# Kernel optimization log

Measured on AMD Instinct MI355X. Metric: run time of the kernel, lower is better.

Reference implementation:

```python
import math
import jax, jax.numpy as jnp
import numpy as np

D = 512
MEM_LEN = 1024
RATIO = 2


def setup_inputs() -> dict:
    key = jax.random.key(0)
    ks = jax.random.split(key, 16)
    s = 1.0 / math.sqrt(D)
    inp = {
        "x": jax.random.normal(ks[0], (4, 2048, D), jnp.float32),
        "fine_mem": jax.random.normal(ks[1], (8, 256, D), jnp.float32),
        "cmem_seq": jax.random.normal(ks[2], (16, 128, D), jnp.float32),
        "comp_query": jax.random.normal(ks[3], (D,), jnp.float32) * 0.02,
        "comp_W": jax.random.normal(ks[4], (D, D), jnp.float32) * s,
        "comp_b": jnp.zeros((D,), jnp.float32),
        "k_W": jax.random.normal(ks[5], (D, D), jnp.float32) * s,
        "k_b": jnp.zeros((D,), jnp.float32),
        "v_W": jax.random.normal(ks[6], (D, D), jnp.float32) * s,
        "v_b": jnp.zeros((D,), jnp.float32),
        "xk_W": jax.random.normal(ks[7], (D, D), jnp.float32) * s,
        "xk_b": jnp.zeros((D,), jnp.float32),
        "ck_W": jax.random.normal(ks[8], (D, D), jnp.float32) * s,
        "ck_b": jnp.zeros((D,), jnp.float32),
        "cv_W": jax.random.normal(ks[9], (D, D), jnp.float32) * s,
        "cv_b": jnp.zeros((D,), jnp.float32),
    }
    return inp


def _compress(combined, comp_query, comp_W, comp_b):
    # AttentionPoolCompressor, vectorized: L tokens -> L//RATIO pooled tokens
    L, d = combined.shape
    L_out = max(L // RATIO, 1)
    c = combined.reshape(L_out, RATIO, d)                      # [L_out, r, d]
    logits = jnp.einsum("d,lrd->lr", comp_query, c) * (d ** -0.5)
    w = jax.nn.softmax(logits, axis=-1)
    pooled = jnp.einsum("lr,lrd->ld", w, c)                    # [L_out, d]
    return pooled @ comp_W + comp_b


def _interp_linear(comp, L):
    # F.interpolate(mode='linear', align_corners=False) along length dim
    L_out = comp.shape[0]
    i = jnp.arange(L, dtype=jnp.float32)
    src = jnp.clip((i + 0.5) * (L_out / L) - 0.5, 0.0, L_out - 1)
    i0 = jnp.floor(src).astype(jnp.int32)
    i1 = jnp.minimum(i0 + 1, L_out - 1)
    frac = (src - i0)[:, None]
    return (1.0 - frac) * comp[i0] + frac * comp[i1]


def reference(x, fine_mem, cmem_seq, comp_query, comp_W, comp_b,
              k_W, k_b, v_W, v_b, xk_W, xk_b, ck_W, ck_b, cv_W, cv_b):
    B, S, d = x.shape
    Nf, Lm, _ = fine_mem.shape
    scale = d ** -0.5

    # keys/values over the ORIGINAL memories (projections precede eviction)
    fine_k = fine_mem @ k_W + k_b      # [Nf, Lm, d]
    fine_v = fine_mem @ v_W + v_b
    cmem_k = cmem_seq @ ck_W + ck_b    # [Nc, Lc, d]
    cmem_v = cmem_seq @ cv_W + cv_b

    # eviction: take leading chunks until cumsum >= mem_len/2 (static)
    K = min(int(math.ceil(0.5 * MEM_LEN / Lm)), Nf)
    combined = fine_mem[:K].reshape(K * Lm, d)                 # [L, d]
    compressed = _compress(combined, comp_query, comp_W, comp_b)
    decoded = _interp_linear(compressed, combined.shape[0])
    recon_loss = jnp.mean((decoded - combined) ** 2)

    # cross-attention over concatenated memory
    query = x @ xk_W + xk_b                                    # [B, S, d]
    mem_k = jnp.concatenate([fine_k.reshape(-1, d), cmem_k.reshape(-1, d)], 0)
    mem_v = jnp.concatenate([fine_v.reshape(-1, d), cmem_v.reshape(-1, d)], 0)
    scores = jnp.einsum("bsd,md->bsm", query, mem_k) * scale   # [B, S, M]
    attn = jax.nn.softmax(scores, axis=-1)
    mem_out = jnp.einsum("bsm,md->bsd", attn, mem_v)
    output = x + mem_out
    return (output, recon_loss)
```

## Files before the change

kernel.cpp:

```cpp
#include <hip/hip_runtime.h>

typedef __attribute__((ext_vector_type(8))) short bf16x8;
typedef __attribute__((ext_vector_type(4))) float f32x4;

#define MFMA16(a,b,c) __builtin_amdgcn_mfma_f32_16x16x32_bf16((a),(b),(c),0,0,0)

__device__ __forceinline__ unsigned short f2bf(float f) {
  unsigned int u = __builtin_bit_cast(unsigned int, f);
  u = (u + 0x7FFFu + ((u >> 16) & 1u)) >> 16;
  return (unsigned short)u;
}
__device__ __forceinline__ float bf2f(unsigned short u) {
  unsigned int v = ((unsigned int)u) << 16;
  return __builtin_bit_cast(float, v);
}
__device__ __forceinline__ unsigned int pack_bf16(float a, float b) {
  return ((unsigned int)f2bf(b) << 16) | (unsigned int)f2bf(a);
}

__global__ __launch_bounds__(256) void wt_transpose5(
    const float* __restrict__ W0, const float* __restrict__ W1,
    const float* __restrict__ W2, const float* __restrict__ W3,
    const float* __restrict__ W4,
    unsigned short* __restrict__ O0, unsigned short* __restrict__ O1,
    unsigned short* __restrict__ O2, unsigned short* __restrict__ O3,
    unsigned short* __restrict__ O4)
{
  const float* W; unsigned short* Wt;
  switch (blockIdx.z) {
    case 0: W = W0; Wt = O0; break;
    case 1: W = W1; Wt = O1; break;
    case 2: W = W2; Wt = O2; break;
    case 3: W = W3; Wt = O3; break;
    default: W = W4; Wt = O4; break;
  }
  __shared__ unsigned short T[32][33];
  int kb = blockIdx.x * 32, nb = blockIdx.y * 32;
  int tx = threadIdx.x & 31, ty = threadIdx.x >> 5;
  #pragma unroll
  for (int s = 0; s < 4; ++s)
    T[ty + 8*s][tx] = f2bf(W[(kb + ty + 8*s)*512 + nb + tx]);
  __syncthreads();
  #pragma unroll
  for (int s = 0; s < 4; ++s)
    Wt[(nb + ty + 8*s)*512 + kb + tx] = T[tx][ty + 8*s];
}

__global__ __launch_bounds__(256) void v_transpose(const unsigned short* __restrict__ V,
    unsigned short* __restrict__ Vt)
{
  __shared__ unsigned short T[32][33];
  int mb = blockIdx.x * 32, db = blockIdx.y * 32;
  int tx = threadIdx.x & 31, ty = threadIdx.x >> 5;
  #pragma unroll
  for (int s = 0; s < 4; ++s)
    T[ty + 8*s][tx] = V[(mb + ty + 8*s)*512 + db + tx];
  __syncthreads();
  #pragma unroll
  for (int s = 0; s < 4; ++s)
    Vt[(db + ty + 8*s)*4096 + mb + tx] = T[tx][ty + 8*s];
}

__global__ __launch_bounds__(256) void proj_all(
    const float* __restrict__ x, const float* __restrict__ fine, const float* __restrict__ cmem,
    const unsigned short* __restrict__ WtXK, const unsigned short* __restrict__ WtK,
    const unsigned short* __restrict__ WtV,  const unsigned short* __restrict__ WtCK,
    const unsigned short* __restrict__ WtCV,
    const float* __restrict__ xkb, const float* __restrict__ kb2, const float* __restrict__ vb2,
    const float* __restrict__ ckb, const float* __restrict__ cvb,
    unsigned short* __restrict__ qry, unsigned short* __restrict__ memk,
    unsigned short* __restrict__ memv)
{
  const float* A; const unsigned short* Bt; const float* bias; unsigned short* C;
  int m0;
  int bx = blockIdx.x;
  if (bx < 64) { A = x; Bt = WtXK; bias = xkb; C = qry; m0 = bx * 128; }
  else {
    int seg = (bx - 64) >> 4;
    m0 = ((bx - 64) & 15) * 128;
    switch (seg) {
      case 0:  A = fine; Bt = WtK;  bias = kb2; C = memk;            break;
      case 1:  A = cmem; Bt = WtCK; bias = ckb; C = memk + 2048*512; break;
      case 2:  A = fine; Bt = WtV;  bias = vb2; C = memv;            break;
      default: A = cmem; Bt = WtCV; bias = cvb; C = memv + 2048*512; break;
    }
  }
  const float cs = (bx < 64) ? 0.04419417382415922f : 1.0f;

  __shared__ unsigned short As[128*32];
  __shared__ unsigned short Bs[64*32];
  const int tid = threadIdx.x;
  const int w = tid >> 6, lane = tid & 63;
  const int lr = lane & 15, lg = lane >> 4;
  const int wm = w >> 1, wn = w & 1;
  const int n0 = blockIdx.y * 64;

  f32x4 acc[4][2];
  #pragma unroll
  for (int mt = 0; mt < 4; ++mt)
    #pragma unroll
    for (int nt = 0; nt < 2; ++nt) acc[mt][nt] = (f32x4){0.f,0.f,0.f,0.f};

  const int arow = tid >> 3, af4 = tid & 7;
  const int brow = tid >> 2, bc8 = tid & 3;

  for (int kb = 0; kb < 512; kb += 32) {
    #pragma unroll
    for (int s = 0; s < 4; ++s) {
      const float4 v = *(const float4*)(A + (m0 + arow + 32*s)*512 + kb + af4*4);
      unsigned long long pk = (unsigned long long)f2bf(v.x)
        | ((unsigned long long)f2bf(v.y) << 16)
        | ((unsigned long long)f2bf(v.z) << 32)
        | ((unsigned long long)f2bf(v.w) << 48);
      *(unsigned long long*)&As[(arow + 32*s)*32 + af4*4] = pk;
    }
    *(int4*)&Bs[brow*32 + bc8*8] = *(const int4*)(Bt + (n0 + brow)*512 + kb + bc8*8);
    __syncthreads();
    bf16x8 af[4], bfr[2];
    #pragma unroll
    for (int mt = 0; mt < 4; ++mt)
      af[mt] = *(const bf16x8*)&As[(wm*64 + mt*16 + lr)*32 + lg*8];
    #pragma unroll
    for (int nt = 0; nt < 2; ++nt)
      bfr[nt] = *(const bf16x8*)&Bs[(wn*32 + nt*16 + lr)*32 + lg*8];
    #pragma unroll
    for (int mt = 0; mt < 4; ++mt)
      #pragma unroll
      for (int nt = 0; nt < 2; ++nt)
        acc[mt][nt] = MFMA16(af[mt], bfr[nt], acc[mt][nt]);
    __syncthreads();
  }
  #pragma unroll
  for (int nt = 0; nt < 2; ++nt) {
    int col = n0 + wn*32 + nt*16 + lr;
    float bv = bias[col];
    #pragma unroll
    for (int mt = 0; mt < 4; ++mt) {
      #pragma unroll
      for (int j = 0; j < 4; ++j) {
        int row = m0 + wm*64 + mt*16 + lg*4 + j;
        C[row*512 + col] = f2bf((acc[mt][nt][j] + bv) * cs);
      }
    }
  }
}

template<int NC>
__global__ __launch_bounds__(256, 2) void attn_kernel(
    const unsigned short* __restrict__ q,
    const unsigned short* __restrict__ mk,
    const unsigned short* __restrict__ vt,
    unsigned short* __restrict__ opart,
    float* __restrict__ mpart,
    float* __restrict__ lpart)
{
  constexpr int CK = 4096 / NC;
  constexpr int ITERS = CK / 64;
  constexpr int PLW = 68;

  __shared__ unsigned short Ks[64*520];
  __shared__ unsigned short Pl[64*PLW];
  __shared__ float Fl[64];
  __shared__ unsigned int Tf[4];

  const int tid = threadIdx.x;
  const int w = tid >> 6, lane = tid & 63;
  const int lr = lane & 15, lg = lane >> 4;
  const int bid = blockIdx.x;
  const int chunk = bid & (NC - 1);
  const int qb = bid / NC;
  const int q0blk = qb * 64;
  const int kvbase = chunk * CK;

  const unsigned short* qgp = q + (size_t)(q0blk + w*16 + lr) * 512 + lg*8;

  f32x4 o[32];
  #pragma unroll
  for (int nt = 0; nt < 32; ++nt) o[nt] = (f32x4){0.f,0.f,0.f,0.f};
  float m = -1e30f, l = 0.f;

  const unsigned short* vgp = vt + (size_t)(w*128 + lr) * 4096 + kvbase + lg*8;

  #define STAGE_K(IT) do {                                                        \
    int kv0_ = kvbase + (IT) * 64;                                                \
    _Pragma("unroll")                                                             \
    for (int i_ = 0; i_ < 16; ++i_) {                                             \
      int r_ = w * 16 + i_;                                                       \
      __builtin_amdgcn_global_load_lds(                                           \
        (const __attribute__((address_space(1))) unsigned int*)                   \
          (mk + (kv0_ + r_)*512 + lane*8),                                        \
        (__attribute__((address_space(3))) unsigned int*)(&Ks[r_*520]), 16, 0, 0);\
    }                                                                             \
  } while (0)

  STAGE_K(0);
  __syncthreads();

  const unsigned short* kp = &Ks[lr * 520];

  for (int it = 0; it < ITERS; ++it) {
    f32x4 t0 = (f32x4){0.f,0.f,0.f,0.f}, t1 = (f32x4){0.f,0.f,0.f,0.f};
    f32x4 t2 = (f32x4){0.f,0.f,0.f,0.f}, t3 = (f32x4){0.f,0.f,0.f,0.f};
    #pragma unroll
    for (int ks = 0; ks < 16; ++ks) {
      bf16x8 qf  = *(const bf16x8*)(qgp + ks*32);
      bf16x8 kb0 = *(const bf16x8*)(kp + ks*32 + lg*8);
      bf16x8 kb1 = *(const bf16x8*)(kp + 16*520 + ks*32 + lg*8);
      bf16x8 kb2 = *(const bf16x8*)(kp + 32*520 + ks*32 + lg*8);
      bf16x8 kb3 = *(const bf16x8*)(kp + 48*520 + ks*32 + lg*8);
      t0 = MFMA16(kb0, qf, t0);
      t1 = MFMA16(kb1, qf, t1);
      t2 = MFMA16(kb2, qf, t2);
      t3 = MFMA16(kb3, qf, t3);
    }

    float pm = fmaxf(fmaxf(fmaxf(t0[0], t0[1]), fmaxf(t0[2], t0[3])),
                     fmaxf(fmaxf(t1[0], t1[1]), fmaxf(t1[2], t1[3])));
    pm = fmaxf(pm, fmaxf(fmaxf(fmaxf(t2[0], t2[1]), fmaxf(t2[2], t2[3])),
                         fmaxf(fmaxf(t3[0], t3[1]), fmaxf(t3[2], t3[3]))));
    pm = fmaxf(pm, __shfl_xor(pm, 16));
    pm = fmaxf(pm, __shfl_xor(pm, 32));

    bool trig = !__all(pm <= m + 8.f);
    if (trig) {
      float mn = fmaxf(m, pm);
      float fl = __expf(m - mn);
      l *= fl;
      m = mn;
      if (lg == 0) Fl[w*16 + lr] = fl;
    }
    if (lane == 0) Tf[w] = trig ? 1u : 0u;

    float p0[4], p1[4], p2[4], p3[4];
    #pragma unroll
    for (int j = 0; j < 4; ++j) {
      p0[j] = __expf(t0[j] - m);
      p1[j] = __expf(t1[j] - m);
      p2[j] = __expf(t2[j] - m);
      p3[j] = __expf(t3[j] - m);
    }
    float rs = ((p0[0]+p0[1]) + (p0[2]+p0[3])) + ((p1[0]+p1[1]) + (p1[2]+p1[3]))
             + ((p2[0]+p2[1]) + (p2[2]+p2[3])) + ((p3[0]+p3[1]) + (p3[2]+p3[3]));
    rs += __shfl_xor(rs, 16);
    rs += __shfl_xor(rs, 32);
    l += rs;

    {
      unsigned short* pr = &Pl[(w*16 + lr)*PLW + lg*4];
      *(uint2*)(pr)      = make_uint2(pack_bf16(p0[0], p0[1]), pack_bf16(p0[2], p0[3]));
      *(uint2*)(pr + 16) = make_uint2(pack_bf16(p1[0], p1[1]), pack_bf16(p1[2], p1[3]));
      *(uint2*)(pr + 32) = make_uint2(pack_bf16(p2[0], p2[1]), pack_bf16(p2[2], p2[3]));
      *(uint2*)(pr + 48) = make_uint2(pack_bf16(p3[0], p3[1]), pack_bf16(p3[2], p3[3]));
    }
    __syncthreads();

    if (it + 1 < ITERS) STAGE_K(it + 1);

    unsigned int tf0 = Tf[0], tf1 = Tf[1], tf2 = Tf[2], tf3 = Tf[3];
    if (tf0 | tf1 | tf2 | tf3) {
      #pragma unroll
      for (int qt = 0; qt < 4; ++qt) {
        unsigned int tfq = (qt == 0) ? tf0 : (qt == 1) ? tf1 : (qt == 2) ? tf2 : tf3;
        if (tfq) {
          f32x4 fq = *(const f32x4*)&Fl[qt*16 + lg*4];
          #pragma unroll
          for (int dt = 0; dt < 8; ++dt) {
            o[qt*8 + dt][0] *= fq[0]; o[qt*8 + dt][1] *= fq[1];
            o[qt*8 + dt][2] *= fq[2]; o[qt*8 + dt][3] *= fq[3];
          }
        }
      }
    }

    const unsigned short* vit = vgp + it*64;
    #pragma unroll
    for (int kvh = 0; kvh < 2; ++kvh) {
      bf16x8 pa[4];
      #pragma unroll
      for (int qt = 0; qt < 4; ++qt)
        pa[qt] = *(const bf16x8*)&Pl[(qt*16 + lr)*PLW + kvh*32 + lg*8];
      #pragma unroll
      for (int dh = 0; dh < 2; ++dh) {
        bf16x8 vb[4];
        #pragma unroll
        for (int dt = 0; dt < 4; ++dt)
          vb[dt] = *(const bf16x8*)(vit + kvh*32 + (size_t)(dh*4 + dt)*16*4096);
        #pragma unroll
        for (int qt = 0; qt < 4; ++qt) {
          #pragma unroll
          for (int dt = 0; dt < 4; ++dt)
            o[qt*8 + dh*4 + dt] = MFMA16(pa[qt], vb[dt], o[qt*8 + dh*4 + dt]);
        }
      }
    }
    __syncthreads();
  }

  unsigned short* ob = opart + (size_t)chunk * 8192 * 512;
  #pragma unroll
  for (int qt = 0; qt < 4; ++qt) {
    #pragma unroll
    for (int dt = 0; dt < 8; ++dt) {
      #pragma unroll
      for (int j = 0; j < 4; ++j) {
        int row = q0blk + qt*16 + lg*4 + j;
        int col = w*128 + dt*16 + lr;
        ob[row*512 + col] = f2bf(o[qt*8 + dt][j]);
      }
    }
  }
  if (lane < 16) {
    mpart[chunk*8192 + q0blk + w*16 + lane] = m;
    lpart[chunk*8192 + q0blk + w*16 + lane] = l;
  }
  #undef STAGE_K
}

template<int NC>
__global__ __launch_bounds__(256) void attn_combine(
    const unsigned short* __restrict__ opart, const float* __restrict__ mpart,
    const float* __restrict__ lpart, const float* __restrict__ x,
    float* __restrict__ out)
{
  int row = blockIdx.x * 4 + (threadIdx.x >> 6);
  int t = threadIdx.x & 63;
  int d0 = t * 8;
  float mc[NC], lc[NC];
  #pragma unroll
  for (int c = 0; c < NC; ++c) { mc[c] = mpart[c*8192 + row]; lc[c] = lpart[c*8192 + row]; }
  float M = mc[0];
  #pragma unroll
  for (int c = 1; c < NC; ++c) M = fmaxf(M, mc[c]);
  float wc[NC], denom = 0.f;
  #pragma unroll
  for (int c = 0; c < NC; ++c) { wc[c] = __expf(mc[c] - M); denom += wc[c] * lc[c]; }
  float inv = 1.0f / denom;
  float acc[8] = {0.f,0.f,0.f,0.f,0.f,0.f,0.f,0.f};
  const unsigned short* base = opart + (size_t)row*512 + d0;
  #pragma unroll
  for (int c = 0; c < NC; ++c) {
    int4 v = *(const int4*)(base + (size_t)c * 8192 * 512);
    const unsigned short* u = (const unsigned short*)&v;
    #pragma unroll
    for (int e = 0; e < 8; ++e) acc[e] += wc[c] * bf2f(u[e]);
  }
  float4 xv0 = *(const float4*)(x + row*512 + d0);
  float4 xv1 = *(const float4*)(x + row*512 + d0 + 4);
  float4 o0, o1;
  o0.x = xv0.x + acc[0]*inv; o0.y = xv0.y + acc[1]*inv;
  o0.z = xv0.z + acc[2]*inv; o0.w = xv0.w + acc[3]*inv;
  o1.x = xv1.x + acc[4]*inv; o1.y = xv1.y + acc[5]*inv;
  o1.z = xv1.z + acc[6]*inv; o1.w = xv1.w + acc[7]*inv;
  *(float4*)(out + row*512 + d0)     = o0;
  *(float4*)(out + row*512 + d0 + 4) = o1;
}

__global__ __launch_bounds__(256) void compress_pool(const float* __restrict__ fine,
    const float* __restrict__ cq, float* __restrict__ pooled, float* __restrict__ loss)
{
  if (blockIdx.x == 0 && threadIdx.x == 0) *loss = 0.f;
  int l = blockIdx.x;
  int t = threadIdx.x;
  const float* c0 = fine + (2*l)*512;
  const float* c1 = c0 + 512;
  float q0 = cq[t], q1 = cq[t+256];
  float a0 = q0*c0[t] + q1*c0[t+256];
  float a1 = q0*c1[t] + q1*c1[t+256];
  #pragma unroll
  for (int m = 1; m < 64; m <<= 1) { a0 += __shfl_xor(a0, m); a1 += __shfl_xor(a1, m); }
  __shared__ float r0[4], r1[4];
  int w = t >> 6;
  if ((t & 63) == 0) { r0[w] = a0; r1[w] = a1; }
  __syncthreads();
  const float sc = 0.04419417382415922f;
  float g0 = (r0[0]+r0[1]+r0[2]+r0[3]) * sc;
  float g1 = (r1[0]+r1[1]+r1[2]+r1[3]) * sc;
  float mx = fmaxf(g0, g1);
  float e0 = __expf(g0-mx), e1 = __expf(g1-mx);
  float inv = 1.0f/(e0+e1);
  float w0 = e0*inv, w1 = e1*inv;
  pooled[l*512 + t]       = w0*c0[t]     + w1*c1[t];
  pooled[l*512 + t + 256] = w0*c0[t+256] + w1*c1[t+256];
}

__global__ __launch_bounds__(256) void comp_gemm(const float* __restrict__ P,
    const float* __restrict__ W, const float* __restrict__ b, float* __restrict__ out)
{
  int gid = blockIdx.x * 256 + threadIdx.x;
  int m = gid >> 9, n = gid & 511;
  const float* a = P + m * 512;
  float acc = b[n];
  #pragma unroll 8
  for (int k = 0; k < 512; ++k) acc += a[k] * W[k*512 + n];
  out[gid] = acc;
}

__global__ __launch_bounds__(256) void interp_loss(const float* __restrict__ comp,
    const float* __restrict__ fine, float* __restrict__ loss)
{
  float acc = 0.f;
  #pragma unroll
  for (int s = 0; s < 4; ++s) {
    int e = blockIdx.x*1024 + s*256 + threadIdx.x;
    int i = e >> 9, d = e & 511;
    float src = fminf(fmaxf((i + 0.5f)*0.5f - 0.5f, 0.f), 255.f);
    int i0 = (int)src;
    int i1 = min(i0 + 1, 255);
    float fr = src - (float)i0;
    float dec = (1.f - fr)*comp[i0*512 + d] + fr*comp[i1*512 + d];
    float df = dec - fine[e];
    acc += df*df;
  }
  #pragma unroll
  for (int m = 1; m < 64; m <<= 1) acc += __shfl_xor(acc, m);
  __shared__ float r[4];
  int w = threadIdx.x >> 6;
  if ((threadIdx.x & 63) == 0) r[w] = acc;
  __syncthreads();
  if (threadIdx.x == 0)
    atomicAdd(loss, (r[0]+r[1]+r[2]+r[3]) * (1.0f/262144.0f));
}

extern "C" void kernel_launch(void* const* d_in, const int* in_sizes, int n_in,
                              void* d_out, int out_size, void* d_ws, size_t ws_size,
                              hipStream_t stream) {
  const float* x     = (const float*)d_in[0];
  const float* fine  = (const float*)d_in[1];
  const float* cmem  = (const float*)d_in[2];
  const float* cq    = (const float*)d_in[3];
  const float* compW = (const float*)d_in[4];
  const float* compb = (const float*)d_in[5];
  const float* kW    = (const float*)d_in[6];
  const float* kb_   = (const float*)d_in[7];
  const float* vW    = (const float*)d_in[8];
  const float* vb_   = (const float*)d_in[9];
  const float* xkW   = (const float*)d_in[10];
  const float* xkb   = (const float*)d_in[11];
  const float* ckW   = (const float*)d_in[12];
  const float* ckb   = (const float*)d_in[13];
  const float* cvW   = (const float*)d_in[14];
  const float* cvb   = (const float*)d_in[15];

  char* ws = (char*)d_ws;
  const size_t WT = 512*512*2;
  unsigned short* WtK  = (unsigned short*)(ws + 0*WT);
  unsigned short* WtV  = (unsigned short*)(ws + 1*WT);
  unsigned short* WtCK = (unsigned short*)(ws + 2*WT);
  unsigned short* WtCV = (unsigned short*)(ws + 3*WT);
  unsigned short* WtXK = (unsigned short*)(ws + 4*WT);
  char* base = ws + 5*WT;
  unsigned short* memk = (unsigned short*)(base);
  unsigned short* memv = (unsigned short*)(base + (4u<<20));
  unsigned short* vt   = (unsigned short*)(base + (8u<<20));
  unsigned short* qry  = (unsigned short*)(base + (12u<<20));
  float* pooled        = (float*)(base + (20u<<20));
  float* comp          = (float*)(base + (20u<<20) + (512u<<10));
  unsigned short* opart= (unsigned short*)(base + (21u<<20));
  float* mpart         = (float*)(base + (21u<<20) + (32ull<<20));
  float* lpart         = mpart + 4*8192;

  float* out  = (float*)d_out;
  float* loss = out + 8192*512;

  wt_transpose5<<<dim3(16,16,5), 256, 0, stream>>>(kW, vW, ckW, cvW, xkW,
                                                   WtK, WtV, WtCK, WtCV, WtXK);

  proj_all<<<dim3(128,8), 256, 0, stream>>>(x, fine, cmem,
      WtXK, WtK, WtV, WtCK, WtCV,
      xkb, kb_, vb_, ckb, cvb,
      qry, memk, memv);

  v_transpose<<<dim3(128,16), 256, 0, stream>>>(memv, vt);

  attn_kernel<4><<<512, 256, 0, stream>>>(qry, memk, vt, opart, mpart, lpart);
  attn_combine<4><<<2048, 256, 0, stream>>>(opart, mpart, lpart, x, out);

  compress_pool<<<256, 256, 0, stream>>>(fine, cq, pooled, loss);
  comp_gemm<<<512, 256, 0, stream>>>(pooled, compW, compb, comp);
  interp_loss<<<256, 256, 0, stream>>>(comp, fine, loss);
}
```

Before: 184.6 us.

## Pre-convert projection inputs to bf16 and stage GEMM tiles via direct LDS loads

A new kernel converts x, fine_mem and cmem_seq to bf16 once, before the projections run. proj_all then reads bf16 A and B tiles with global_load_lds straight into shared memory instead of loading fp32 and converting per tile. This removes the repeated fp32 loads and conversions across the 8 N-blocks, at the cost of an extra launch and an extra bf16 round-trip through memory. The attention kernel also raises wave priority around its MFMA loops with s_setprio, aiming for better overlap of compute with memory.

```diff
diff --git a/kernel.cpp b/kernel.cpp
--- a/kernel.cpp
+++ b/kernel.cpp
@@ -16,6 +16,23 @@
 }
 __device__ __forceinline__ unsigned int pack_bf16(float a, float b) {
   return ((unsigned int)f2bf(b) << 16) | (unsigned int)f2bf(a);
+}
+
+__global__ __launch_bounds__(256) void cvt_bf16_all(
+    const float* __restrict__ x, const float* __restrict__ fine,
+    const float* __restrict__ cmem, unsigned short* __restrict__ abf)
+{
+  size_t off = ((size_t)blockIdx.x * 256 + threadIdx.x) * 4;
+  const float* src;
+  if (off < (size_t)8192*512)        src = x + off;
+  else if (off < (size_t)10240*512)  src = fine + (off - (size_t)8192*512);
+  else                               src = cmem + (off - (size_t)10240*512);
+  float4 v = *(const float4*)src;
+  unsigned long long pk = (unsigned long long)f2bf(v.x)
+    | ((unsigned long long)f2bf(v.y) << 16)
+    | ((unsigned long long)f2bf(v.z) << 32)
+    | ((unsigned long long)f2bf(v.w) << 48);
+  *(unsigned long long*)(abf + off) = pk;
 }
 
 __global__ __launch_bounds__(256) void wt_transpose5(
@@ -62,7 +79,7 @@
 }
 
 __global__ __launch_bounds__(256) void proj_all(
-    const float* __restrict__ x, const float* __restrict__ fine, const float* __restrict__ cmem,
+    const unsigned short* __restrict__ abf,
     const unsigned short* __restrict__ WtXK, const unsigned short* __restrict__ WtK,
     const unsigned short* __restrict__ WtV,  const unsigned short* __restrict__ WtCK,
     const unsigned short* __restrict__ WtCV,
@@ -71,18 +88,18 @@
     unsigned short* __restrict__ qry, unsigned short* __restrict__ memk,
     unsigned short* __restrict__ memv)
 {
-  const float* A; const unsigned short* Bt; const float* bias; unsigned short* C;
+  const unsigned short* A; const unsigned short* Bt; const float* bias; unsigned short* C;
   int m0;
   int bx = blockIdx.x;
-  if (bx < 64) { A = x; Bt = WtXK; bias = xkb; C = qry; m0 = bx * 128; }
+  if (bx < 64) { A = abf; Bt = WtXK; bias = xkb; C = qry; m0 = bx * 128; }
   else {
     int seg = (bx - 64) >> 4;
     m0 = ((bx - 64) & 15) * 128;
     switch (seg) {
-      case 0:  A = fine; Bt = WtK;  bias = kb2; C = memk;            break;
-      case 1:  A = cmem; Bt = WtCK; bias = ckb; C = memk + 2048*512; break;
-      case 2:  A = fine; Bt = WtV;  bias = vb2; C = memv;            break;
-      default: A = cmem; Bt = WtCV; bias = cvb; C = memv + 2048*512; break;
+      case 0:  A = abf + (size_t)8192*512;  Bt = WtK;  bias = kb2; C = memk;            break;
+      case 1:  A = abf + (size_t)10240*512; Bt = WtCK; bias = ckb; C = memk + 2048*512; break;
+      case 2:  A = abf + (size_t)8192*512;  Bt = WtV;  bias = vb2; C = memv;            break;
+      default: A = abf + (size_t)10240*512; Bt = WtCV; bias = cvb; C = memv + 2048*512; break;
     }
   }
   const float cs = (bx < 64) ? 0.04419417382415922f : 1.0f;
@@ -101,20 +118,25 @@
     #pragma unroll
     for (int nt = 0; nt < 2; ++nt) acc[mt][nt] = (f32x4){0.f,0.f,0.f,0.f};
 
-  const int arow = tid >> 3, af4 = tid & 7;
-  const int brow = tid >> 2, bc8 = tid & 3;
+  const int arow = lane >> 2;
+  const int acol = (lane & 3) * 8;
 
   for (int kb = 0; kb < 512; kb += 32) {
     #pragma unroll
-    for (int s = 0; s < 4; ++s) {
-      const float4 v = *(const float4*)(A + (m0 + arow + 32*s)*512 + kb + af4*4);
-      unsigned long long pk = (unsigned long long)f2bf(v.x)
-        | ((unsigned long long)f2bf(v.y) << 16)
-        | ((unsigned long long)f2bf(v.z) << 32)
-        | ((unsigned long long)f2bf(v.w) << 48);
-      *(unsigned long long*)&As[(arow + 32*s)*32 + af4*4] = pk;
-    }
-    *(int4*)&Bs[brow*32 + bc8*8] = *(const int4*)(Bt + (n0 + brow)*512 + kb + bc8*8);
+    for (int j = 0; j < 2; ++j) {
+      int r0 = (w*2 + j) * 16;
+      __builtin_amdgcn_global_load_lds(
+        (const __attribute__((address_space(1))) unsigned int*)
+          (A + (size_t)(m0 + r0 + arow)*512 + kb + acol),
+        (__attribute__((address_space(3))) unsigned int*)(&As[r0*32]), 16, 0, 0);
+    }
+    {
+      int r0 = w * 16;
+      __builtin_amdgcn_global_load_lds(
+        (const __attribute__((address_space(1))) unsigned int*)
+          (Bt + (size_t)(n0 + r0 + arow)*512 + kb + acol),
+        (__attribute__((address_space(3))) unsigned int*)(&Bs[r0*32]), 16, 0, 0);
+    }
     __syncthreads();
     bf16x8 af[4], bfr[2];
     #pragma unroll
@@ -201,6 +223,7 @@
   for (int it = 0; it < ITERS; ++it) {
     f32x4 t0 = (f32x4){0.f,0.f,0.f,0.f}, t1 = (f32x4){0.f,0.f,0.f,0.f};
     f32x4 t2 = (f32x4){0.f,0.f,0.f,0.f}, t3 = (f32x4){0.f,0.f,0.f,0.f};
+    __builtin_amdgcn_s_setprio(1);
     #pragma unroll
     for (int ks = 0; ks < 16; ++ks) {
       bf16x8 qf  = *(const bf16x8*)(qgp + ks*32);
@@ -213,6 +236,7 @@
       t2 = MFMA16(kb2, qf, t2);
       t3 = MFMA16(kb3, qf, t3);
     }
+    __builtin_amdgcn_s_setprio(0);
 
     float pm = fmaxf(fmaxf(fmaxf(t0[0], t0[1]), fmaxf(t0[2], t0[3])),
                      fmaxf(fmaxf(t1[0], t1[1]), fmaxf(t1[2], t1[3])));
@@ -285,12 +309,14 @@
         #pragma unroll
         for (int dt = 0; dt < 4; ++dt)
           vb[dt] = *(const bf16x8*)(vit + kvh*32 + (size_t)(dh*4 + dt)*16*4096);
+        __builtin_amdgcn_s_setprio(1);
         #pragma unroll
         for (int qt = 0; qt < 4; ++qt) {
           #pragma unroll
           for (int dt = 0; dt < 4; ++dt)
             o[qt*8 + dh*4 + dt] = MFMA16(pa[qt], vb[dt], o[qt*8 + dh*4 + dt]);
         }
+        __builtin_amdgcn_s_setprio(0);
       }
     }
     __syncthreads();
@@ -458,14 +484,17 @@
   unsigned short* opart= (unsigned short*)(base + (21u<<20));
   float* mpart         = (float*)(base + (21u<<20) + (32ull<<20));
   float* lpart         = mpart + 4*8192;
+  unsigned short* abf  = (unsigned short*)(base + (54u<<20));
 
   float* out  = (float*)d_out;
   float* loss = out + 8192*512;
 
+  cvt_bf16_all<<<6144, 256, 0, stream>>>(x, fine, cmem, abf);
+
   wt_transpose5<<<dim3(16,16,5), 256, 0, stream>>>(kW, vW, ckW, cvW, xkW,
                                                    WtK, WtV, WtCK, WtCV, WtXK);
 
-  proj_all<<<dim3(128,8), 256, 0, stream>>>(x, fine, cmem,
+  proj_all<<<dim3(128,8), 256, 0, stream>>>(abf,
       WtXK, WtK, WtV, WtCK, WtCV,
       xkb, kb_, vb_, ckb, cvb,
       qry, memk, memv);
```

Result: no change. 186.7 us (+1.1%).
